# Performance work log

Hardware: AMD Instinct MI355X
Metric: run time of the kernel (lower is better)

Reference implementation:

```python
import jax, jax.numpy as jnp
import numpy as np

B, S, D, H = 4, 2048, 1024, 16
DH = D // H


def setup_inputs() -> dict:
    key = jax.random.key(0)
    ks = jax.random.split(key, 12)
    s = 0.02
    inp = {
        "q": jax.random.normal(ks[0], (B, S, D), jnp.float32),
        "k": jax.random.normal(ks[1], (B, S, D), jnp.float32),
        "v": jax.random.normal(ks[2], (B, S, D), jnp.float32),
        # causal mask, broadcastable over batch and heads (mask==0 -> -1e9)
        "mask": jnp.tril(jnp.ones((S, S), jnp.int32))[None, None, :, :],
        "wq": jax.random.normal(ks[3], (D, D), jnp.float32) * s,
        "bq": jnp.zeros((D,), jnp.float32),
        "wk": jax.random.normal(ks[4], (D, D), jnp.float32) * s,
        "bk": jnp.zeros((D,), jnp.float32),
        "wv": jax.random.normal(ks[5], (D, D), jnp.float32) * s,
        "bv": jnp.zeros((D,), jnp.float32),
        "wo": jax.random.normal(ks[6], (D, D), jnp.float32) * s,
        "bo": jnp.zeros((D,), jnp.float32),
    }
    return inp


def reference(q, k, v, mask, wq, bq, wk, bk, wv, bv, wo, bo):
    # linear projections (torch Linear: x @ W^T + b)
    qh = (q @ wq.T + bq).reshape(B, S, H, DH).transpose(0, 2, 1, 3)  # [B,H,S,DH]
    kh = (k @ wk.T + bk).reshape(B, S, H, DH).transpose(0, 2, 1, 3)
    vh = (v @ wv.T + bv).reshape(B, S, H, DH).transpose(0, 2, 1, 3)
    scale = 1.0 / jnp.sqrt(jnp.float32(DH))
    score = jnp.einsum("bhqd,bhkd->bhqk", qh, kh) * scale  # [B,H,S,S]
    score = jnp.where(mask == 0, jnp.float32(-1e9), score)
    attn = jax.nn.softmax(score, axis=-1)
    ctx = jnp.einsum("bhqk,bhkd->bhqd", attn, vh)  # [B,H,S,DH]
    ctx = ctx.transpose(0, 2, 1, 3).reshape(B, S, D)
    return ctx @ wo.T + bo
```

## Files before the change

kernel.cpp:

```cpp
#include <hip/hip_runtime.h>
#include <hip/hip_bf16.h>

#define NB 4
#define NS 2048
#define ND 1024
#define NH 16
#define NDH 64
#define E_ 8388608
#define W_ 1048576

typedef __attribute__((ext_vector_type(8))) __bf16 bf16x8;
typedef __attribute__((ext_vector_type(4))) float f32x4;
typedef __attribute__((ext_vector_type(2))) unsigned int u32x2;
typedef unsigned short us16;
typedef unsigned int u32;

__device__ __forceinline__ unsigned short f2bf(float f) {
  union { float f; unsigned u; } v; v.f = f;
  unsigned r = v.u + 0x7FFFu + ((v.u >> 16) & 1u);
  return (unsigned short)(r >> 16);
}

typedef const __attribute__((address_space(1))) unsigned int* gas_t;
typedef __attribute__((address_space(3))) unsigned int* las_t;
__device__ __forceinline__ void gl2lds16(const void* g, void* l) {
  __builtin_amdgcn_global_load_lds((gas_t)g, (las_t)l, 16, 0, 0);
}

__global__ __launch_bounds__(256) void conv_bf16(
    const float* __restrict__ q, const float* __restrict__ k, const float* __restrict__ v,
    const float* __restrict__ wq, const float* __restrict__ wk, const float* __restrict__ wv,
    const float* __restrict__ wo,
    us16* __restrict__ qb, us16* __restrict__ kb, us16* __restrict__ vb,
    us16* __restrict__ wqb, us16* __restrict__ wkb, us16* __restrict__ wvb,
    us16* __restrict__ wob)
{
  int b = blockIdx.x;
  int seg, off;
  if (b < 24576) { seg = b >> 13; off = b & 8191; }
  else { b -= 24576; seg = 3 + (b >> 10); off = b & 1023; }
  const float* s; us16* d;
  switch (seg) {
    case 0: s = q;  d = qb;  break;
    case 1: s = k;  d = kb;  break;
    case 2: s = v;  d = vb;  break;
    case 3: s = wq; d = wqb; break;
    case 4: s = wk; d = wkb; break;
    case 5: s = wv; d = wvb; break;
    default: s = wo; d = wob; break;
  }
  size_t idx = ((size_t)off * 256 + threadIdx.x) * 4;
  float4 f = *(const float4*)(s + idx);
  ushort4 u;
  u.x = f2bf(f.x); u.y = f2bf(f.y); u.z = f2bf(f.z); u.w = f2bf(f.w);
  *(ushort4*)(d + idx) = u;
}

#define STG(bi, kt) { \
    gl2lds16(ga + (kt),             &As[bi][w * 32][0]); \
    gl2lds16(ga + (kt) + 16 * ND,   &As[bi][w * 32 + 16][0]); \
    gl2lds16(gb + (kt),             &Bs[bi][w * 16][0]); }

#define BARX() { __builtin_amdgcn_s_barrier(); \
                 __builtin_amdgcn_sched_barrier(0); \
                 asm volatile("" ::: "memory"); }

#define GEMM8_PIPE() \
  f32x4 acc[4][4] = {}; \
  STG(0, 0) STG(1, 32) STG(2, 64) \
  asm volatile("s_waitcnt vmcnt(6)" ::: "memory"); \
  BARX() \
  _Pragma("unroll") \
  for (int t = 0; t < 32; ++t) { \
    if (t + 3 < 32) STG((t + 3) & 3, (t + 3) * 32) \
    bf16x8 af[4], bfr[4]; \
    _Pragma("unroll") \
    for (int i = 0; i < 4; ++i) \
      af[i] = *(const bf16x8*)&As[t & 3][wm * 64 + i * 16 + l15][(quad ^ (l15 & 3)) * 8]; \
    _Pragma("unroll") \
    for (int j = 0; j < 4; ++j) \
      bfr[j] = *(const bf16x8*)&Bs[t & 3][wn * 64 + j * 16 + l15][(quad ^ (l15 & 3)) * 8]; \
    __builtin_amdgcn_s_setprio(1); \
    _Pragma("unroll") \
    for (int i = 0; i < 4; ++i) \
      _Pragma("unroll") \
      for (int j = 0; j < 4; ++j) \
        acc[i][j] = __builtin_amdgcn_mfma_f32_16x16x32_bf16(af[i], bfr[j], acc[i][j], 0, 0, 0); \
    __builtin_amdgcn_s_setprio(0); \
    if (t < 29)       asm volatile("s_waitcnt vmcnt(6)" ::: "memory"); \
    else if (t == 29) asm volatile("s_waitcnt vmcnt(3)" ::: "memory"); \
    else if (t == 30) asm volatile("s_waitcnt vmcnt(0)" ::: "memory"); \
    if (t < 31) BARX() \
  }

__global__ __launch_bounds__(512, 2) void gemm_proj8(
    const us16* __restrict__ A0, const us16* __restrict__ A1, const us16* __restrict__ A2,
    const us16* __restrict__ W0, const us16* __restrict__ W1, const us16* __restrict__ W2,
    const float* __restrict__ b0, const float* __restrict__ b1, const float* __restrict__ b2,
    us16* __restrict__ o0, us16* __restrict__ o1, us16* __restrict__ o2,
    float qscale, int s0, int s1, int s2)
{
  const int seg = (blockIdx.z == 0) ? s0 : (blockIdx.z == 1) ? s1 : s2;
  const us16* A  = (blockIdx.z == 0) ? A0 : (blockIdx.z == 1) ? A1 : A2;
  const us16* Wt = (blockIdx.z == 0) ? W0 : (blockIdx.z == 1) ? W1 : W2;
  const float* bias = (blockIdx.z == 0) ? b0 : (blockIdx.z == 1) ? b1 : b2;
  us16* out = (blockIdx.z == 0) ? o0 : (blockIdx.z == 1) ? o1 : o2;
  const float scale = (seg == 0) ? qscale : 1.0f;

  __shared__ us16 As[4][256][32];
  __shared__ us16 Bs[4][128][32];
  const int tid = threadIdx.x;
  const int lane = tid & 63;
  const int w = tid >> 6;
  const int l15 = lane & 15, quad = lane >> 4;
  const int lr4 = lane >> 2;
  const int cu4 = (lane & 3) ^ (lr4 & 3);
  const int wm = w >> 1, wn = w & 1;
  const int rowBase = blockIdx.x * 256, colBase = blockIdx.y * 128;
  const us16* ga = A  + (size_t)(rowBase + w * 32 + lr4) * ND + cu4 * 8;
  const us16* gb = Wt + (size_t)(colBase + w * 16 + lr4) * ND + cu4 * 8;

  GEMM8_PIPE()

  const int wr = wm * 64, wc = wn * 64;
  if (seg < 2) {
    #pragma unroll
    for (int i = 0; i < 4; ++i) {
      #pragma unroll
      for (int j = 0; j < 4; ++j) {
        int colg = colBase + wc + j * 16 + l15;
        float bval = bias[colg];
        #pragma unroll
        for (int r = 0; r < 4; ++r) {
          int rowg = rowBase + wr + i * 16 + quad * 4 + r;
          out[(size_t)rowg * ND + colg] = f2bf((acc[i][j][r] + bval) * scale);
        }
      }
    }
  } else {
    #pragma unroll
    for (int i = 0; i < 4; ++i) {
      #pragma unroll
      for (int j = 0; j < 4; ++j) {
        int colg = colBase + wc + j * 16 + l15;
        float bval = bias[colg];
        int h_ = colg >> 6, d_ = colg & 63;
        int rowg0 = rowBase + wr + i * 16 + quad * 4;
        int b_ = rowg0 >> 11, sr0 = rowg0 & (NS - 1);
        ushort4 vv;
        vv.x = f2bf(acc[i][j][0] + bval);
        vv.y = f2bf(acc[i][j][1] + bval);
        vv.z = f2bf(acc[i][j][2] + bval);
        vv.w = f2bf(acc[i][j][3] + bval);
        *(ushort4*)(out + ((size_t)(b_ * NH + h_) * NDH + d_) * NS + sr0) = vv;
      }
    }
  }
}

__global__ __launch_bounds__(512, 2) void gemm_out8(
    const us16* __restrict__ A, const us16* __restrict__ Wt,
    const float* __restrict__ bias, float* __restrict__ out)
{
  __shared__ us16 As[4][256][32];
  __shared__ us16 Bs[4][128][32];
  const int tid = threadIdx.x;
  const int lane = tid & 63;
  const int w = tid >> 6;
  const int l15 = lane & 15, quad = lane >> 4;
  const int lr4 = lane >> 2;
  const int cu4 = (lane & 3) ^ (lr4 & 3);
  const int wm = w >> 1, wn = w & 1;
  const int rowBase = blockIdx.x * 256, colBase = blockIdx.y * 128;
  const us16* ga = A  + (size_t)(rowBase + w * 32 + lr4) * ND + cu4 * 8;
  const us16* gb = Wt + (size_t)(colBase + w * 16 + lr4) * ND + cu4 * 8;

  GEMM8_PIPE()

  const int wr = wm * 64, wc = wn * 64;
  #pragma unroll
  for (int i = 0; i < 4; ++i) {
    #pragma unroll
    for (int j = 0; j < 4; ++j) {
      int colg = colBase + wc + j * 16 + l15;
      float bval = bias[colg];
      #pragma unroll
      for (int r = 0; r < 4; ++r) {
        int rowg = rowBase + wr + i * 16 + quad * 4 + r;
        out[(size_t)rowg * ND + colg] = acc[i][j][r] + bval;
      }
    }
  }
}

__global__ __launch_bounds__(256, 2) void attn(
    const us16* __restrict__ Qh, const us16* __restrict__ Kh,
    const us16* __restrict__ Vht, us16* __restrict__ ctx)
{
  __shared__ us16 Ks[2][128][64];
  __shared__ us16 Vts[2][64][128];
  __shared__ us16 Ps[4][32][32];
  us16* Qsta = &Vts[1][0][0];

  const int bh = blockIdx.x & 63;
  const int pr = blockIdx.x >> 6;
  const int b_ = bh >> 4, h_ = bh & 15;
  const int tid = threadIdx.x, lane = tid & 63, w = tid >> 6;
  const int l15 = lane & 15, quad = lane >> 4;
  const int sw = l15 & 7;
  const int lr8 = lane >> 3;
  const int cu = (lane & 7) ^ (lr8 & 7);
  const int vr = lane >> 4;
  const int vs = lane & 15;
  const int cs0 = (vs & 8) | ((vs & 7) ^ vr);
  const int cs1 = (vs & 8) | ((vs & 7) ^ (vr | 4));

  bf16x8 ones;
  #pragma unroll
  for (int i = 0; i < 8; ++i) ones[i] = (__bf16)1.0f;

  const us16* gk  = Kh  + ((size_t)b_ * NS + w * 32 + lr8) * ND + h_ * NDH + cu * 8;
  const us16* gv0 = Vht + ((size_t)bh * NDH + w * 16 + vr) * NS + cs0 * 8;
  const us16* gv1 = Vht + ((size_t)bh * NDH + w * 16 + 4 + vr) * NS + cs1 * 8;

  for (int pass = 0; pass < 2; ++pass) {
    const int tq = pass ? (15 - pr) : pr;
    const int qb0 = tq * 128;
    const int nt = tq + 1;
    const int qw = qb0 + w * 32;

    __syncthreads();
    {
      const us16* gq = Qh + ((size_t)b_ * NS + qb0 + w * 32 + lr8) * ND + h_ * NDH + cu * 8;
      #pragma unroll
      for (int u = 0; u < 4; ++u)
        gl2lds16(gq + (size_t)u * 8 * ND, Qsta + (w * 32 + u * 8) * 64);
    }
    #pragma unroll
    for (int u = 0; u < 4; ++u)
      gl2lds16(gk + (size_t)(u * 8) * ND, &Ks[0][w * 32 + u * 8][0]);
    gl2lds16(gv0,          &Vts[0][w * 16][0]);
    gl2lds16(gv1,          &Vts[0][w * 16 + 4][0]);
    gl2lds16(gv0 + 8 * NS, &Vts[0][w * 16 + 8][0]);
    gl2lds16(gv1 + 8 * NS, &Vts[0][w * 16 + 12][0]);
    __syncthreads();
    bf16x8 bq[2][2];
    #pragma unroll
    for (int ntl = 0; ntl < 2; ++ntl)
      #pragma unroll
      for (int c = 0; c < 2; ++c)
        bq[ntl][c] = *(const bf16x8*)(Qsta + (w * 32 + ntl * 16 + l15) * 64 +
                                      (((c * 4 + quad) ^ sw) * 8));

    f32x4 o[2][4] = {};
    f32x4 o_l[2] = {};

    for (int it = 0; it < nt; ++it) {
      const int kb = it * 128;
      const int cur = it & 1;
      __syncthreads();
      if (it + 1 < nt) {
        const int nxt = cur ^ 1;
        const int kn = kb + 128;
        #pragma unroll
        for (int u = 0; u < 4; ++u)
          gl2lds16(gk + (size_t)(kn + u * 8) * ND, &Ks[nxt][w * 32 + u * 8][0]);
        gl2lds16(gv0 + kn,          &Vts[nxt][w * 16][0]);
        gl2lds16(gv1 + kn,          &Vts[nxt][w * 16 + 4][0]);
        gl2lds16(gv0 + kn + 8 * NS, &Vts[nxt][w * 16 + 8][0]);
        gl2lds16(gv1 + kn + 8 * NS, &Vts[nxt][w * 16 + 12][0]);
      }
      #pragma unroll
      for (int h2 = 0; h2 < 4; ++h2) {
        const int keyb0 = kb + h2 * 32;
        if (keyb0 > qw + 31) continue;
        const bool full = (keyb0 + 31 <= qw);
        f32x4 s[2][2];
        __builtin_amdgcn_s_setprio(1);
        #pragma unroll
        for (int mt = 0; mt < 2; ++mt) {
          bf16x8 ak0 = *(const bf16x8*)&Ks[cur][h2 * 32 + mt * 16 + l15][(quad ^ sw) * 8];
          bf16x8 ak1 = *(const bf16x8*)&Ks[cur][h2 * 32 + mt * 16 + l15][((4 + quad) ^ sw) * 8];
          #pragma unroll
          for (int ntl = 0; ntl < 2; ++ntl) {
            f32x4 t = {};
            t = __builtin_amdgcn_mfma_f32_16x16x32_bf16(ak0, bq[ntl][0], t, 0, 0, 0);
            t = __builtin_amdgcn_mfma_f32_16x16x32_bf16(ak1, bq[ntl][1], t, 0, 0, 0);
            s[mt][ntl] = t;
          }
        }
        __builtin_amdgcn_s_setprio(0);
        #pragma unroll
        for (int mt = 0; mt < 2; ++mt)
          #pragma unroll
          for (int ntl = 0; ntl < 2; ++ntl) {
            u32 u[4];
            if (full) {
              #pragma unroll
              for (int r = 0; r < 4; ++r)
                u[r] = __float_as_uint(__builtin_amdgcn_exp2f(s[mt][ntl][r]));
            } else {
              const int keyb = keyb0 + mt * 16 + quad * 4;
              const int qg = qw + ntl * 16 + l15;
              #pragma unroll
              for (int r = 0; r < 4; ++r) {
                float p = (keyb + r <= qg) ? __builtin_amdgcn_exp2f(s[mt][ntl][r]) : 0.f;
                u[r] = __float_as_uint(p);
              }
            }
            u32 lo = (u[0] >> 16) | (u[1] & 0xffff0000u);
            u32 hi = (u[2] >> 16) | (u[3] & 0xffff0000u);
            int uswz = (mt * 2 + (quad >> 1)) ^ (l15 & 3);
            *(u32x2*)&Ps[w][ntl * 16 + l15][uswz * 8 + (quad & 1) * 4] = (u32x2){lo, hi};
          }
        bf16x8 bv[4];
        #pragma unroll
        for (int n = 0; n < 4; ++n)
          bv[n] = *(const bf16x8*)&Vts[cur][n * 16 + l15][((h2 * 4 + quad) ^ sw) * 8];
        __builtin_amdgcn_s_setprio(1);
        #pragma unroll
        for (int ntl = 0; ntl < 2; ++ntl) {
          bf16x8 ap = *(const bf16x8*)&Ps[w][ntl * 16 + l15][(quad ^ (l15 & 3)) * 8];
          o_l[ntl] = __builtin_amdgcn_mfma_f32_16x16x32_bf16(ap, ones, o_l[ntl], 0, 0, 0);
          #pragma unroll
          for (int n = 0; n < 4; ++n)
            o[ntl][n] = __builtin_amdgcn_mfma_f32_16x16x32_bf16(ap, bv[n], o[ntl][n], 0, 0, 0);
        }
        __builtin_amdgcn_s_setprio(0);
      }
    }

    #pragma unroll
    for (int ntl = 0; ntl < 2; ++ntl) {
      #pragma unroll
      for (int r = 0; r < 4; ++r) {
        float inv = __builtin_amdgcn_rcpf(o_l[ntl][r]);
        int qg = qb0 + w * 32 + ntl * 16 + quad * 4 + r;
        us16* dst = ctx + ((size_t)b_ * NS + qg) * ND + h_ * NDH;
        #pragma unroll
        for (int n = 0; n < 4; ++n)
          dst[n * 16 + l15] = f2bf(o[ntl][n][r] * inv);
      }
    }
  }
}

extern "C" void kernel_launch(void* const* d_in, const int* in_sizes, int n_in,
                              void* d_out, int out_size, void* d_ws, size_t ws_size,
                              hipStream_t stream) {
  const float* q  = (const float*)d_in[0];
  const float* k  = (const float*)d_in[1];
  const float* v  = (const float*)d_in[2];
  const float* wq = (const float*)d_in[4];
  const float* bq_ = (const float*)d_in[5];
  const float* wk = (const float*)d_in[6];
  const float* bk_ = (const float*)d_in[7];
  const float* wv = (const float*)d_in[8];
  const float* bv_ = (const float*)d_in[9];
  const float* wo = (const float*)d_in[10];
  const float* bo_ = (const float*)d_in[11];

  us16* ws = (us16*)d_ws;
  us16* qb  = ws;
  us16* kb  = ws + (size_t)E_;
  us16* vb  = ws + (size_t)2 * E_;
  us16* wqb = ws + (size_t)3 * E_;
  us16* wkb = wqb + W_;
  us16* wvb = wkb + W_;
  us16* wob = wvb + W_;
  us16* KhF = wob + W_;
  us16* ctx = vb;
  us16* Vht = (us16*)d_out;
  us16* Qh  = (us16*)d_out + (size_t)E_;

  const float qscale = 0.125f * 1.44269504088896340736f;
  const bool fused = ws_size >= ((size_t)4 * E_ + 4 * W_) * 2;

  conv_bf16<<<28672, 256, 0, stream>>>(q, k, v, wq, wk, wv, wo,
                                       qb, kb, vb, wqb, wkb, wvb, wob);
  if (fused) {
    gemm_proj8<<<dim3(32, 8, 3), 512, 0, stream>>>(
        qb, kb, vb, wqb, wkb, wvb, bq_, bk_, bv_, Qh, KhF, Vht, qscale, 0, 1, 2);
    attn<<<512, 256, 0, stream>>>(Qh, KhF, Vht, ctx);
  } else {
    gemm_proj8<<<dim3(32, 8, 2), 512, 0, stream>>>(
        qb, vb, vb, wqb, wvb, wvb, bq_, bv_, bv_, Qh, Vht, Vht, qscale, 0, 2, 2);
    gemm_proj8<<<dim3(32, 8, 1), 512, 0, stream>>>(
        kb, kb, kb, wkb, wkb, wkb, bk_, bk_, bk_, qb, qb, qb, qscale, 1, 1, 1);
    attn<<<512, 256, 0, stream>>>(Qh, qb, Vht, ctx);
  }
  gemm_out8<<<dim3(32, 8), 512, 0, stream>>>(ctx, wob, bo_, (float*)d_out);
}
```

Baseline: 326.4 us.

## Use 4-wave GEMM blocks with 128x64 warp tiles and triple-buffered LDS

The projection and output GEMMs now run 256 threads per block instead of 512, and each wave computes a 128x64 output tile (8x4 MFMAs) instead of 64x64. The LDS pipeline goes from 4 stages with 3-ahead prefetch to 3 stages with 2-ahead prefetch, and the swizzle pattern is changed. The aim is more MFMA work per LDS fragment load and less LDS use per block. In exchange each wave holds twice the accumulator registers, which may lower occupancy, and the shallower prefetch gives less room to hide memory latency.

```diff
diff --git a/kernel.cpp b/kernel.cpp
--- a/kernel.cpp
+++ b/kernel.cpp
@@ -56,44 +56,46 @@
   *(ushort4*)(d + idx) = u;
 }
 
-#define STG(bi, kt) { \
-    gl2lds16(ga + (kt),             &As[bi][w * 32][0]); \
-    gl2lds16(ga + (kt) + 16 * ND,   &As[bi][w * 32 + 16][0]); \
-    gl2lds16(gb + (kt),             &Bs[bi][w * 16][0]); }
+#define STG3(bi, kt) { \
+    gl2lds16(gaS + (kt),            &As[bi][w * 64][0]); \
+    gl2lds16(gaS + (kt) + 16 * ND,  &As[bi][w * 64 + 16][0]); \
+    gl2lds16(gaS + (kt) + 32 * ND,  &As[bi][w * 64 + 32][0]); \
+    gl2lds16(gaS + (kt) + 48 * ND,  &As[bi][w * 64 + 48][0]); \
+    gl2lds16(gbS + (kt),            &Bs[bi][w * 32][0]); \
+    gl2lds16(gbS + (kt) + 16 * ND,  &Bs[bi][w * 32 + 16][0]); }
 
 #define BARX() { __builtin_amdgcn_s_barrier(); \
                  __builtin_amdgcn_sched_barrier(0); \
                  asm volatile("" ::: "memory"); }
 
-#define GEMM8_PIPE() \
-  f32x4 acc[4][4] = {}; \
-  STG(0, 0) STG(1, 32) STG(2, 64) \
+#define GEMM_PIPE3() \
+  f32x4 acc[8][4] = {}; \
+  STG3(0, 0) STG3(1, 32) \
   asm volatile("s_waitcnt vmcnt(6)" ::: "memory"); \
   BARX() \
   _Pragma("unroll") \
   for (int t = 0; t < 32; ++t) { \
-    if (t + 3 < 32) STG((t + 3) & 3, (t + 3) * 32) \
-    bf16x8 af[4], bfr[4]; \
+    if (t + 2 < 32) STG3((t + 2) % 3, (t + 2) * 32) \
+    bf16x8 af[8], bfr[4]; \
     _Pragma("unroll") \
-    for (int i = 0; i < 4; ++i) \
-      af[i] = *(const bf16x8*)&As[t & 3][wm * 64 + i * 16 + l15][(quad ^ (l15 & 3)) * 8]; \
+    for (int i = 0; i < 8; ++i) \
+      af[i] = *(const bf16x8*)&As[t % 3][wm * 128 + i * 16 + l15][ps]; \
     _Pragma("unroll") \
     for (int j = 0; j < 4; ++j) \
-      bfr[j] = *(const bf16x8*)&Bs[t & 3][wn * 64 + j * 16 + l15][(quad ^ (l15 & 3)) * 8]; \
+      bfr[j] = *(const bf16x8*)&Bs[t % 3][wn * 64 + j * 16 + l15][ps]; \
     __builtin_amdgcn_s_setprio(1); \
     _Pragma("unroll") \
-    for (int i = 0; i < 4; ++i) \
+    for (int i = 0; i < 8; ++i) \
       _Pragma("unroll") \
       for (int j = 0; j < 4; ++j) \
         acc[i][j] = __builtin_amdgcn_mfma_f32_16x16x32_bf16(af[i], bfr[j], acc[i][j], 0, 0, 0); \
     __builtin_amdgcn_s_setprio(0); \
-    if (t < 29)       asm volatile("s_waitcnt vmcnt(6)" ::: "memory"); \
-    else if (t == 29) asm volatile("s_waitcnt vmcnt(3)" ::: "memory"); \
+    if (t < 30)       asm volatile("s_waitcnt vmcnt(6)" ::: "memory"); \
     else if (t == 30) asm volatile("s_waitcnt vmcnt(0)" ::: "memory"); \
     if (t < 31) BARX() \
   }
 
-__global__ __launch_bounds__(512, 2) void gemm_proj8(
+__global__ __launch_bounds__(256, 2) void gemm_proj9(
     const us16* __restrict__ A0, const us16* __restrict__ A1, const us16* __restrict__ A2,
     const us16* __restrict__ W0, const us16* __restrict__ W1, const us16* __restrict__ W2,
     const float* __restrict__ b0, const float* __restrict__ b1, const float* __restrict__ b2,
@@ -107,25 +109,26 @@
   us16* out = (blockIdx.z == 0) ? o0 : (blockIdx.z == 1) ? o1 : o2;
   const float scale = (seg == 0) ? qscale : 1.0f;
 
-  __shared__ us16 As[4][256][32];
-  __shared__ us16 Bs[4][128][32];
+  __shared__ us16 As[3][256][32];
+  __shared__ us16 Bs[3][128][32];
   const int tid = threadIdx.x;
   const int lane = tid & 63;
   const int w = tid >> 6;
   const int l15 = lane & 15, quad = lane >> 4;
-  const int lr4 = lane >> 2;
-  const int cu4 = (lane & 3) ^ (lr4 & 3);
   const int wm = w >> 1, wn = w & 1;
+  const int ps = (quad ^ ((l15 >> 1) & 3)) * 8;
+  const int sr4 = lane >> 2;
+  const int sc  = (lane & 3) ^ ((lane >> 3) & 3);
   const int rowBase = blockIdx.x * 256, colBase = blockIdx.y * 128;
-  const us16* ga = A  + (size_t)(rowBase + w * 32 + lr4) * ND + cu4 * 8;
-  const us16* gb = Wt + (size_t)(colBase + w * 16 + lr4) * ND + cu4 * 8;
-
-  GEMM8_PIPE()
-
-  const int wr = wm * 64, wc = wn * 64;
+  const us16* gaS = A  + (size_t)(rowBase + w * 64 + sr4) * ND + sc * 8;
+  const us16* gbS = Wt + (size_t)(colBase + w * 32 + sr4) * ND + sc * 8;
+
+  GEMM_PIPE3()
+
+  const int wr = wm * 128, wc = wn * 64;
   if (seg < 2) {
     #pragma unroll
-    for (int i = 0; i < 4; ++i) {
+    for (int i = 0; i < 8; ++i) {
       #pragma unroll
       for (int j = 0; j < 4; ++j) {
         int colg = colBase + wc + j * 16 + l15;
@@ -139,7 +142,7 @@
     }
   } else {
     #pragma unroll
-    for (int i = 0; i < 4; ++i) {
+    for (int i = 0; i < 8; ++i) {
       #pragma unroll
       for (int j = 0; j < 4; ++j) {
         int colg = colBase + wc + j * 16 + l15;
@@ -158,28 +161,29 @@
   }
 }
 
-__global__ __launch_bounds__(512, 2) void gemm_out8(
+__global__ __launch_bounds__(256, 2) void gemm_out9(
     const us16* __restrict__ A, const us16* __restrict__ Wt,
     const float* __restrict__ bias, float* __restrict__ out)
 {
-  __shared__ us16 As[4][256][32];
-  __shared__ us16 Bs[4][128][32];
+  __shared__ us16 As[3][256][32];
+  __shared__ us16 Bs[3][128][32];
   const int tid = threadIdx.x;
   const int lane = tid & 63;
   const int w = tid >> 6;
   const int l15 = lane & 15, quad = lane >> 4;
-  const int lr4 = lane >> 2;
-  const int cu4 = (lane & 3) ^ (lr4 & 3);
   const int wm = w >> 1, wn = w & 1;
+  const int ps = (quad ^ ((l15 >> 1) & 3)) * 8;
+  const int sr4 = lane >> 2;
+  const int sc  = (lane & 3) ^ ((lane >> 3) & 3);
   const int rowBase = blockIdx.x * 256, colBase = blockIdx.y * 128;
-  const us16* ga = A  + (size_t)(rowBase + w * 32 + lr4) * ND + cu4 * 8;
-  const us16* gb = Wt + (size_t)(colBase + w * 16 + lr4) * ND + cu4 * 8;
-
-  GEMM8_PIPE()
-
-  const int wr = wm * 64, wc = wn * 64;
+  const us16* gaS = A  + (size_t)(rowBase + w * 64 + sr4) * ND + sc * 8;
+  const us16* gbS = Wt + (size_t)(colBase + w * 32 + sr4) * ND + sc * 8;
+
+  GEMM_PIPE3()
+
+  const int wr = wm * 128, wc = wn * 64;
   #pragma unroll
-  for (int i = 0; i < 4; ++i) {
+  for (int i = 0; i < 8; ++i) {
     #pragma unroll
     for (int j = 0; j < 4; ++j) {
       int colg = colBase + wc + j * 16 + l15;
@@ -379,15 +383,15 @@
   conv_bf16<<<28672, 256, 0, stream>>>(q, k, v, wq, wk, wv, wo,
                                        qb, kb, vb, wqb, wkb, wvb, wob);
   if (fused) {
-    gemm_proj8<<<dim3(32, 8, 3), 512, 0, stream>>>(
+    gemm_proj9<<<dim3(32, 8, 3), 256, 0, stream>>>(
         qb, kb, vb, wqb, wkb, wvb, bq_, bk_, bv_, Qh, KhF, Vht, qscale, 0, 1, 2);
     attn<<<512, 256, 0, stream>>>(Qh, KhF, Vht, ctx);
   } else {
-    gemm_proj8<<<dim3(32, 8, 2), 512, 0, stream>>>(
+    gemm_proj9<<<dim3(32, 8, 2), 256, 0, stream>>>(
         qb, vb, vb, wqb, wvb, wvb, bq_, bv_, bv_, Qh, Vht, Vht, qscale, 0, 2, 2);
-    gemm_proj8<<<dim3(32, 8, 1), 512, 0, stream>>>(
+    gemm_proj9<<<dim3(32, 8, 1), 256, 0, stream>>>(
         kb, kb, kb, wkb, wkb, wkb, bk_, bk_, bk_, qb, qb, qb, qscale, 1, 1, 1);
     attn<<<512, 256, 0, stream>>>(Qh, qb, Vht, ctx);
   }
-  gemm_out8<<<dim3(32, 8), 512, 0, stream>>>(ctx, wob, bo_, (float*)d_out);
-}
+  gemm_out9<<<dim3(32, 8), 256, 0, stream>>>(ctx, wob, bo_, (float*)d_out);
+}
```

New measurement: 330.8 us. Within noise of the previous version (+1.4%).
